# Kernel optimization log

Hardware: AMD Instinct MI355X
Metric: run time of the kernel (lower is better)

## Reference

```python
import jax, jax.numpy as jnp
import numpy as np

N_NODES = 100000


def sage_conv(x, src, dst, W_l, b_l, W_r):
    # PyG SAGEConv (aggr='mean'): out = lin_l(mean_j x_j) + lin_r(x_i)
    msg = x[src]  # [E, d] gather of source-node features
    agg = jax.ops.segment_sum(msg, dst, num_segments=N_NODES)  # [N, d]
    deg = jax.ops.segment_sum(jnp.ones((src.shape[0],), x.dtype), dst,
                              num_segments=N_NODES)
    mean = agg / jnp.clip(deg, 1.0, None)[:, None]
    return mean @ W_l.T + b_l + x @ W_r.T


def setup_inputs() -> dict:
    key = jax.random.key(0)
    ks = jax.random.split(key, 12)
    d_in, d_h, d_out, n_edges = 64, 64, 2, 1200000
    s = 1.0 / np.sqrt(d_h)
    inp = {
        "x": jax.random.normal(ks[0], (N_NODES, d_in), dtype=jnp.float32),
        "edge_index": jax.random.randint(ks[1], (2, n_edges), 0, N_NODES,
                                         dtype=jnp.int64),
        "W_l1": jax.random.uniform(ks[2], (d_h, d_in), jnp.float32, -s, s),
        "b_l1": jax.random.uniform(ks[3], (d_h,), jnp.float32, -s, s),
        "W_r1": jax.random.uniform(ks[4], (d_h, d_in), jnp.float32, -s, s),
        "W_l2": jax.random.uniform(ks[5], (d_h, d_h), jnp.float32, -s, s),
        "b_l2": jax.random.uniform(ks[6], (d_h,), jnp.float32, -s, s),
        "W_r2": jax.random.uniform(ks[7], (d_h, d_h), jnp.float32, -s, s),
        "W_c": jax.random.uniform(ks[8], (d_out, d_h), jnp.float32, -s, s),
        "b_c": jax.random.uniform(ks[9], (d_out,), jnp.float32, -s, s),
    }
    return inp


def reference(x, edge_index, W_l1, b_l1, W_r1, W_l2, b_l2, W_r2, W_c, b_c):
    src, dst = edge_index[0], edge_index[1]
    # layer 1 + relu (dropout is identity in eval mode)
    h = jax.nn.relu(sage_conv(x, src, dst, W_l1, b_l1, W_r1))
    # layer 2 (no relu per forward())
    h = sage_conv(h, src, dst, W_l2, b_l2, W_r2)
    # classifier
    return h @ W_c.T + b_c
```

## Files before the change

### kernel.cpp

```cpp
#include <hip/hip_runtime.h>

#define N_NODES 100000
#define D 64
#define NTILES 3125
#define NBUCK 391
#define NBLK_A 256
#define GCNT_N (NBUCK * NBLK_A)
#define NCHUNK ((GCNT_N + 255) / 256)
#define NTILE_T (N_NODES / 32)
#define TROW 72
#define TBLK 512

typedef __attribute__((ext_vector_type(8))) short short8;
typedef __attribute__((ext_vector_type(16))) float f32x16;
union Pack8 { uint4 u; short8 s; };

__device__ __forceinline__ unsigned f2bf(float f) {
  unsigned u = __float_as_uint(f);
  return (u + 0x7fffu + ((u >> 16) & 1u)) >> 16;
}
#define BF_LO(u) __uint_as_float(((unsigned)(u)) << 16)
#define BF_HI(u) __uint_as_float(((unsigned)(u)) & 0xffff0000u)


__global__ __launch_bounds__(256) void passA_count(const int* __restrict__ dst,
                                                   int* __restrict__ gcnt,
                                                   int nE, int ec) {
  __shared__ int cnt[NBUCK];
  int t = threadIdx.x, blk = blockIdx.x;
  for (int i = t; i < NBUCK; i += 256) cnt[i] = 0;
  __syncthreads();
  int e0 = blk * ec, e1 = min(e0 + ec, nE);
  for (int e = e0 + t; e < e1; e += 256) atomicAdd(&cnt[dst[e] >> 8], 1);
  __syncthreads();
  for (int b = t; b < NBUCK; b += 256) gcnt[b * NBLK_A + blk] = cnt[b];
}

__global__ void gscan_p1(const int* __restrict__ g, int* __restrict__ csum) {
  int t = threadIdx.x, b = blockIdx.x;
  int i = b * 256 + t;
  int v = (i < GCNT_N) ? g[i] : 0;
  for (int off = 32; off; off >>= 1) v += __shfl_down(v, off);
  __shared__ int ws4[4];
  if ((t & 63) == 0) ws4[t >> 6] = v;
  __syncthreads();
  if (t == 0) csum[b] = ws4[0] + ws4[1] + ws4[2] + ws4[3];
}

__global__ void gscan_p2(int* __restrict__ csum, int nB) {
  __shared__ int s[1024];
  int t = threadIdx.x;
  int orig = (t < nB) ? csum[t] : 0;
  s[t] = orig;
  __syncthreads();
  for (int off = 1; off < 1024; off <<= 1) {
    int v = (t >= off) ? s[t - off] : 0;
    __syncthreads();
    s[t] += v;
    __syncthreads();
  }
  if (t < nB) csum[t] = s[t] - orig;
}

__global__ void gscan_p3(int* __restrict__ g, const int* __restrict__ csum) {
  __shared__ int s[256];
  int t = threadIdx.x, b = blockIdx.x;
  int i = b * 256 + t;
  int d = (i < GCNT_N) ? g[i] : 0;
  s[t] = d;
  __syncthreads();
  for (int off = 1; off < 256; off <<= 1) {
    int v = (t >= off) ? s[t - off] : 0;
    __syncthreads();
    s[t] += v;
    __syncthreads();
  }
  if (i < GCNT_N) g[i] = s[t] - d + csum[b];
}

__global__ __launch_bounds__(256) void passC_prep(
    const int* __restrict__ src, const int* __restrict__ dst,
    const int* __restrict__ S, uint2* __restrict__ pairs, int nE, int ec,
    const float* __restrict__ Wc, const float* __restrict__ Wl2,
    const float* __restrict__ Wr2, const float* __restrict__ bl2,
    const float* __restrict__ bc, const float* __restrict__ Wl1,
    const float* __restrict__ Wr1, float* __restrict__ A2,
    float* __restrict__ B2, float* __restrict__ bfv,
    unsigned short* __restrict__ wcat) {
  __shared__ int cur[NBUCK];
  int t = threadIdx.x, blk = blockIdx.x;
  if (blk < NBLK_A) {
    for (int b = t; b < NBUCK; b += 256) cur[b] = S[b * NBLK_A + blk];
    __syncthreads();
    int e0 = blk * ec, e1 = min(e0 + ec, nE);
    for (int e = e0 + t; e < e1; e += 256) {
      int d = dst[e];
      int p = atomicAdd(&cur[d >> 8], 1);
      pairs[p] = make_uint2((unsigned)d, (unsigned)src[e]);
    }
  } else {
    for (int i = t; i < 8192; i += 256)
      wcat[i] = (unsigned short)f2bf((i < 4096) ? Wl1[i] : Wr1[i - 4096]);
    if (t < 128) {
      int c = t >> 6, k = t & 63;
      float sa = 0.f, sb = 0.f;
      for (int j = 0; j < 64; ++j) {
        float w = Wc[c * 64 + j];
        sa = fmaf(w, Wl2[j * 64 + k], sa);
        sb = fmaf(w, Wr2[j * 64 + k], sb);
      }
      A2[c * 64 + k] = sa;
      B2[c * 64 + k] = sb;
    }
    if (t < 2) {
      float s = bc[t];
      for (int j = 0; j < 64; ++j) s = fmaf(Wc[t * 64 + j], bl2[j], s);
      bfv[t] = s;
    }
  }
}

__global__ __launch_bounds__(256) void passD_transform(
    const uint2* __restrict__ pairs, const int* __restrict__ S,
    int* __restrict__ rowstart, int* __restrict__ degI,
    uint2* __restrict__ srt, int nE,
    const float* __restrict__ x, const unsigned short* __restrict__ wcat,
    const float* __restrict__ bl, unsigned short* __restrict__ t1,
    unsigned short* __restrict__ r1b) {
  __shared__ int lh[256];
  __shared__ int sc[256];
  __shared__ int cur[256];
  int t = threadIdx.x;
  if (blockIdx.x < NBUCK) {
    int b = blockIdx.x;
    int base = S[b * NBLK_A];
    int end = (b == NBUCK - 1) ? nE : S[(b + 1) * NBLK_A];
    lh[t] = 0;
    __syncthreads();
    for (int p = base + t; p < end; p += 256) atomicAdd(&lh[pairs[p].x & 255], 1);
    __syncthreads();
    int d = lh[t];
    sc[t] = d;
    __syncthreads();
    for (int off = 1; off < 256; off <<= 1) {
      int v = (t >= off) ? sc[t - off] : 0;
      __syncthreads();
      sc[t] += v;
      __syncthreads();
    }
    int ex = sc[t] - d;
    int node = b * 256 + t;
    if (node < N_NODES) {
      rowstart[node] = base + ex;
      degI[node] = d;
    }
    cur[t] = base + ex;
    __syncthreads();
    for (int p = base + t; p < end; p += 256) {
      uint2 e = pairs[p];
      int slot = atomicAdd(&cur[e.x & 255], 1);
      srt[slot] = e;
    }
  } else {
    int lane = t & 63;
    int l31 = lane & 31, hi = lane >> 5;

    short8 af[4][4];
#pragma unroll
    for (int jt = 0; jt < 4; ++jt)
#pragma unroll
      for (int kk = 0; kk < 4; ++kk)
        af[jt][kk] =
            *(const short8*)(wcat + (jt * 32 + l31) * 64 + kk * 16 + 8 * hi);

    const f32x16 Z = {0.f, 0.f, 0.f, 0.f, 0.f, 0.f, 0.f, 0.f,
                      0.f, 0.f, 0.f, 0.f, 0.f, 0.f, 0.f, 0.f};
    const float4* x4 = (const float4*)x;

    int gw = ((blockIdx.x - NBUCK) * 256 + t) >> 6;
    int nW = (TBLK * 256) >> 6;

    for (int tile = gw; tile < NTILE_T; tile += nW) {
      int node = tile * 32 + l31;
      f32x16 acc[4] = {Z, Z, Z, Z};
#pragma unroll
      for (int kk = 0; kk < 4; ++kk) {
        float4 fa = x4[(size_t)node * 16 + kk * 4 + 2 * hi];
        float4 fb = x4[(size_t)node * 16 + kk * 4 + 2 * hi + 1];
        Pack8 pk;
        pk.u.x = f2bf(fa.x) | (f2bf(fa.y) << 16);
        pk.u.y = f2bf(fa.z) | (f2bf(fa.w) << 16);
        pk.u.z = f2bf(fb.x) | (f2bf(fb.y) << 16);
        pk.u.w = f2bf(fb.z) | (f2bf(fb.w) << 16);
        acc[0] = __builtin_amdgcn_mfma_f32_32x32x16_bf16(af[0][kk], pk.s, acc[0], 0, 0, 0);
        acc[1] = __builtin_amdgcn_mfma_f32_32x32x16_bf16(af[1][kk], pk.s, acc[1], 0, 0, 0);
        acc[2] = __builtin_amdgcn_mfma_f32_32x32x16_bf16(af[2][kk], pk.s, acc[2], 0, 0, 0);
        acc[3] = __builtin_amdgcn_mfma_f32_32x32x16_bf16(af[3][kk], pk.s, acc[3], 0, 0, 0);
      }
#pragma unroll
      for (int jt = 0; jt < 2; ++jt)
#pragma unroll
        for (int rg = 0; rg < 4; ++rg) {
          int j0 = jt * 32 + 8 * rg + 4 * hi;
          uint2 p;
          p.x = f2bf(acc[jt][4 * rg + 0]) | (f2bf(acc[jt][4 * rg + 1]) << 16);
          p.y = f2bf(acc[jt][4 * rg + 2]) | (f2bf(acc[jt][4 * rg + 3]) << 16);
          *(uint2*)(t1 + (size_t)node * 64 + j0) = p;
        }
#pragma unroll
      for (int jt = 2; jt < 4; ++jt)
#pragma unroll
        for (int rg = 0; rg < 4; ++rg) {
          int j0 = (jt - 2) * 32 + 8 * rg + 4 * hi;
          float4 bv = ((const float4*)bl)[j0 >> 2];
          uint2 p;
          p.x = f2bf(acc[jt][4 * rg + 0] + bv.x) |
                (f2bf(acc[jt][4 * rg + 1] + bv.y) << 16);
          p.y = f2bf(acc[jt][4 * rg + 2] + bv.z) |
                (f2bf(acc[jt][4 * rg + 3] + bv.w) << 16);
          *(uint2*)(r1b + (size_t)node * 64 + j0) = p;
        }
    }
  }
}

__global__ __launch_bounds__(256) void tile_g1(
    const uint2* __restrict__ srt, const int* __restrict__ rowstart,
    const unsigned short* __restrict__ t1,
    const unsigned short* __restrict__ r1b, const float* __restrict__ A2,
    const float* __restrict__ B2, float2* __restrict__ g2,
    float2* __restrict__ s2, int nE) {
  __shared__ float pAB[4][64];
  __shared__ unsigned short stg[4][2][16 * TROW];
  __shared__ int ideg[4][64];
  int t = threadIdx.x, lane = t & 63, w = t >> 6;
  pAB[t >> 6][t & 63] = (t < 128) ? A2[t] : B2[t - 128];
  __syncthreads();

  int tile = blockIdx.x;
  int base = rowstart[tile * 32];
  int end = (tile == NTILES - 1) ? nE : rowstart[(tile + 1) * 32];
  int l31 = lane & 31, hi = lane >> 5;
  int o = lane >> 3, j8 = lane & 7;
  unsigned short* stA = &stg[w][0][0];
  unsigned short* stB = &stg[w][1][0];

  int ngAll = (end > base) ? ((end - base + 15) >> 4) : 0;
  int gper = (ngAll + 3) >> 2;
  int wbase = base + min(w * gper, ngAll) * 16;
  int wend = min(base + min((w + 1) * gper, ngAll) * 16, end);

  const f32x16 Z = {0.f, 0.f, 0.f, 0.f, 0.f, 0.f, 0.f, 0.f,
                    0.f, 0.f, 0.f, 0.f, 0.f, 0.f, 0.f, 0.f};
  f32x16 acc0 = Z, acc1 = Z;
  int degc = 0;
  int ng = (wend > wbase) ? ((wend - wbase + 15) >> 4) : 0;

  uint2 prA = make_uint2(0u, 0u), prB = make_uint2(0u, 0u);
  int cntA = 0, cntB = 0;
  uint4 vA0 = make_uint4(0, 0, 0, 0), vA1 = vA0, vB0 = vA0, vB1 = vA0;
  if (ng > 0) {
    prA = srt[min(wbase + (lane & 15), nE - 1)];
    cntA = min(wend - wbase, 16);
    int s0 = __shfl((int)prA.y, o), s1 = __shfl((int)prA.y, 8 + o);
    vA0 = *(const uint4*)(t1 + (size_t)((o < cntA) ? s0 : 0) * 64 + j8 * 8);
    vA1 = *(const uint4*)(t1 + (size_t)((8 + o < cntA) ? s1 : 0) * 64 + j8 * 8);
  }
  if (ng > 1) {
    int nb = wbase + 16;
    prB = srt[min(nb + (lane & 15), nE - 1)];
    cntB = min(wend - nb, 16);
    int s0 = __shfl((int)prB.y, o), s1 = __shfl((int)prB.y, 8 + o);
    vB0 = *(const uint4*)(t1 + (size_t)((o < cntB) ? s0 : 0) * 64 + j8 * 8);
    vB1 = *(const uint4*)(t1 + (size_t)((8 + o < cntB) ? s1 : 0) * 64 + j8 * 8);
  }

  for (int gg = 0; gg < ng; gg += 2) {
    bool hasB = (gg + 1 < ng);
    *(uint4*)(stA + o * TROW + j8 * 8) = vA0;
    *(uint4*)(stA + (8 + o) * TROW + j8 * 8) = vA1;
    if (hasB) {
      *(uint4*)(stB + o * TROW + j8 * 8) = vB0;
      *(uint4*)(stB + (8 + o) * TROW + j8 * 8) = vB1;
    }
    unsigned amA[8], amB[8];
#pragma unroll
    for (int m = 0; m < 8; ++m) {
      int e = 8 * hi + m;
      int dv = __shfl((int)prA.x, e);
      bool ok = (e < cntA) && ((dv & 31) == l31);
      amA[m] = ok ? 0x3F80u : 0u;
      degc += (amA[m] >> 7) & 1;
    }
    if (hasB) {
#pragma unroll
      for (int m = 0; m < 8; ++m) {
        int e = 8 * hi + m;
        int dv = __shfl((int)prB.x, e);
        bool ok = (e < cntB) && ((dv & 31) == l31);
        amB[m] = ok ? 0x3F80u : 0u;
        degc += (amB[m] >> 7) & 1;
      }
    }
    if (gg + 2 < ng) {
      int nb = wbase + (gg + 2) * 16;
      prA = srt[min(nb + (lane & 15), nE - 1)];
      cntA = min(wend - nb, 16);
      int s0 = __shfl((int)prA.y, o), s1 = __shfl((int)prA.y, 8 + o);
      vA0 = *(const uint4*)(t1 + (size_t)((o < cntA) ? s0 : 0) * 64 + j8 * 8);
      vA1 = *(const uint4*)(t1 + (size_t)((8 + o < cntA) ? s1 : 0) * 64 + j8 * 8);
    }
    if (gg + 3 < ng) {
      int nb = wbase + (gg + 3) * 16;
      prB = srt[min(nb + (lane & 15), nE - 1)];
      cntB = min(wend - nb, 16);
      int s0 = __shfl((int)prB.y, o), s1 = __shfl((int)prB.y, 8 + o);
      vB0 = *(const uint4*)(t1 + (size_t)((o < cntB) ? s0 : 0) * 64 + j8 * 8);
      vB1 = *(const uint4*)(t1 + (size_t)((8 + o < cntB) ? s1 : 0) * 64 + j8 * 8);
    }
    {
      Pack8 I;
      I.u.x = amA[0] | (amA[1] << 16);
      I.u.y = amA[2] | (amA[3] << 16);
      I.u.z = amA[4] | (amA[5] << 16);
      I.u.w = amA[6] | (amA[7] << 16);
      unsigned short b0[8], b1[8];
#pragma unroll
      for (int m = 0; m < 8; ++m) {
        b0[m] = stA[(8 * hi + m) * TROW + l31];
        b1[m] = stA[(8 * hi + m) * TROW + 32 + l31];
      }
      Pack8 F0, F1;
      F0.u.x = b0[0] | ((unsigned)b0[1] << 16);
      F0.u.y = b0[2] | ((unsigned)b0[3] << 16);
      F0.u.z = b0[4] | ((unsigned)b0[5] << 16);
      F0.u.w = b0[6] | ((unsigned)b0[7] << 16);
      F1.u.x = b1[0] | ((unsigned)b1[1] << 16);
      F1.u.y = b1[2] | ((unsigned)b1[3] << 16);
      F1.u.z = b1[4] | ((unsigned)b1[5] << 16);
      F1.u.w = b1[6] | ((unsigned)b1[7] << 16);
      acc0 = __builtin_amdgcn_mfma_f32_32x32x16_bf16(F0.s, I.s, acc0, 0, 0, 0);
      acc1 = __builtin_amdgcn_mfma_f32_32x32x16_bf16(F1.s, I.s, acc1, 0, 0, 0);
    }
    if (hasB) {
      Pack8 I;
      I.u.x = amB[0] | (amB[1] << 16);
      I.u.y = amB[2] | (amB[3] << 16);
      I.u.z = amB[4] | (amB[5] << 16);
      I.u.w = amB[6] | (amB[7] << 16);
      unsigned short b0[8], b1[8];
#pragma unroll
      for (int m = 0; m < 8; ++m) {
        b0[m] = stB[(8 * hi + m) * TROW + l31];
        b1[m] = stB[(8 * hi + m) * TROW + 32 + l31];
      }
      Pack8 F0, F1;
      F0.u.x = b0[0] | ((unsigned)b0[1] << 16);
      F0.u.y = b0[2] | ((unsigned)b0[3] << 16);
      F0.u.z = b0[4] | ((unsigned)b0[5] << 16);
      F0.u.w = b0[6] | ((unsigned)b0[7] << 16);
      F1.u.x = b1[0] | ((unsigned)b1[1] << 16);
      F1.u.y = b1[2] | ((unsigned)b1[3] << 16);
      F1.u.z = b1[4] | ((unsigned)b1[5] << 16);
      F1.u.w = b1[6] | ((unsigned)b1[7] << 16);
      acc0 = __builtin_amdgcn_mfma_f32_32x32x16_bf16(F0.s, I.s, acc0, 0, 0, 0);
      acc1 = __builtin_amdgcn_mfma_f32_32x32x16_bf16(F1.s, I.s, acc1, 0, 0, 0);
    }
  }

  ideg[w][lane] = degc;
  __syncthreads();
  float* red = (float*)&stg[0][0][0];
  for (int r = 1; r < 4; ++r) {
    if (w == r) {
#pragma unroll
      for (int i = 0; i < 16; ++i) {
        red[i * 64 + lane] = acc0[i];
        red[(16 + i) * 64 + lane] = acc1[i];
      }
    }
    __syncthreads();
    if (w == 0) {
#pragma unroll
      for (int i = 0; i < 16; ++i) {
        acc0[i] += red[i * 64 + lane];
        acc1[i] += red[(16 + i) * 64 + lane];
      }
    }
    __syncthreads();
  }

  if (w == 0) {
    int dtot = ideg[0][lane] + ideg[1][lane] + ideg[2][lane] + ideg[3][lane];
    float degf = (float)(dtot + __shfl_xor(dtot, 32));
    float inv = 1.f / fmaxf(degf, 1.f);
    int node = tile * 32 + l31;
    float d0 = 0.f, d1 = 0.f, d2 = 0.f, d3 = 0.f;
#pragma unroll
    for (int fb = 0; fb < 2; ++fb) {
#pragma unroll
      for (int q4 = 0; q4 < 4; ++q4) {
        int f0 = fb * 32 + q4 * 8 + 4 * hi;
        uint2 rv = *(const uint2*)(r1b + (size_t)node * 64 + f0);
        float bias[4] = {BF_LO(rv.x), BF_HI(rv.x), BF_LO(rv.y), BF_HI(rv.y)};
#pragma unroll
        for (int j = 0; j < 4; ++j) {
          float a = fb ? acc1[q4 * 4 + j] : acc0[q4 * 4 + j];
          float hv = fmaxf(fmaf(a, inv, bias[j]), 0.f);
          int f = f0 + j;
          d0 = fmaf(hv, pAB[0][f], d0);
          d1 = fmaf(hv, pAB[1][f], d1);
          d2 = fmaf(hv, pAB[2][f], d2);
          d3 = fmaf(hv, pAB[3][f], d3);
        }
      }
    }
    d0 += __shfl_xor(d0, 32);
    d1 += __shfl_xor(d1, 32);
    d2 += __shfl_xor(d2, 32);
    d3 += __shfl_xor(d3, 32);
    if (hi == 0) {
      g2[node] = make_float2(d0, d1);
      s2[node] = make_float2(d2, d3);
    }
  }
}

__global__ __launch_bounds__(256) void gather2_kernel(
    const int* __restrict__ rowstart, const int* __restrict__ degI,
    const uint2* __restrict__ srt, const float2* __restrict__ g2,
    const float2* __restrict__ s2, const float* __restrict__ bfv,
    float* __restrict__ out, int nE) {
  int tid = threadIdx.x, lane = tid & 63;
  int q = lane >> 4, l16 = lane & 15;
  float bf0 = bfv[0], bf1 = bfv[1];
  int gq = ((blockIdx.x * 256 + tid) >> 6) * 4 + q;
  int strideN = ((gridDim.x * 256) >> 6) * 4;
  for (int n = gq; n < N_NODES; n += strideN) {
    int rs = rowstart[n], dg = degI[n];
    float s0 = 0.f, s1 = 0.f;
    for (int base = 0; base < dg; base += 16) {
      int e = base + l16;
      int a = (int)srt[min(rs + ((e < dg) ? e : 0), nE - 1)].y;
      float2 v = g2[a];
      float m = (e < dg) ? 1.f : 0.f;
      s0 = fmaf(v.x, m, s0);
      s1 = fmaf(v.y, m, s1);
    }
    s0 += __shfl_xor(s0, 1); s0 += __shfl_xor(s0, 2);
    s0 += __shfl_xor(s0, 4); s0 += __shfl_xor(s0, 8);
    s1 += __shfl_xor(s1, 1); s1 += __shfl_xor(s1, 2);
    s1 += __shfl_xor(s1, 4); s1 += __shfl_xor(s1, 8);
    if (l16 == 0) {
      float inv = 1.f / (float)max(dg, 1);
      float2 sv = s2[n];
      out[(size_t)n * 2 + 0] = fmaf(s0, inv, sv.x) + bf0;
      out[(size_t)n * 2 + 1] = fmaf(s1, inv, sv.y) + bf1;
    }
  }
}

extern "C" void kernel_launch(void* const* d_in, const int* in_sizes, int n_in,
                              void* d_out, int out_size, void* d_ws,
                              size_t ws_size, hipStream_t stream) {
  const float* x   = (const float*)d_in[0];
  const int*   ei  = (const int*)d_in[1];
  const float* Wl1 = (const float*)d_in[2];
  const float* bl1 = (const float*)d_in[3];
  const float* Wr1 = (const float*)d_in[4];
  const float* Wl2 = (const float*)d_in[5];
  const float* bl2 = (const float*)d_in[6];
  const float* Wr2 = (const float*)d_in[7];
  const float* Wc  = (const float*)d_in[8];
  const float* bc  = (const float*)d_in[9];
  float* out = (float*)d_out;

  int nE = in_sizes[1] / 2;
  const int* src = ei;
  const int* dst = ei + nE;

  uint2* pairs = (uint2*)d_ws;
  uint2* srt = pairs + nE;
  unsigned short* t1 = (unsigned short*)(srt + nE);
  unsigned short* r1b = t1 + (size_t)N_NODES * D;
  float2* g2 = (float2*)(r1b + (size_t)N_NODES * D);
  float2* s2 = g2 + N_NODES;
  float* A2 = (float*)(s2 + N_NODES);
  float* B2 = A2 + 128;
  float* bfv = B2 + 128;
  unsigned short* wcat = (unsigned short*)(bfv + 4);
  int* degI = (int*)(wcat + 8192);
  int* rowstart = degI + N_NODES;
  int* gcnt = rowstart + N_NODES;
  int* csum = gcnt + GCNT_N;

  int ec = (nE + NBLK_A - 1) / NBLK_A;

  passA_count<<<NBLK_A, 256, 0, stream>>>(dst, gcnt, nE, ec);
  gscan_p1<<<NCHUNK, 256, 0, stream>>>(gcnt, csum);
  gscan_p2<<<1, 1024, 0, stream>>>(csum, NCHUNK);
  gscan_p3<<<NCHUNK, 256, 0, stream>>>(gcnt, csum);
  passC_prep<<<NBLK_A + 1, 256, 0, stream>>>(src, dst, gcnt, pairs, nE, ec,
                                             Wc, Wl2, Wr2, bl2, bc, Wl1, Wr1,
                                             A2, B2, bfv, wcat);
  passD_transform<<<NBUCK + TBLK, 256, 0, stream>>>(pairs, gcnt, rowstart,
                                                    degI, srt, nE, x, wcat,
                                                    bl1, t1, r1b);
  tile_g1<<<NTILES, 256, 0, stream>>>(srt, rowstart, t1, r1b, A2, B2, g2, s2,
                                      nE);
  gather2_kernel<<<512, 256, 0, stream>>>(rowstart, degI, srt, g2, s2, bfv,
                                          out, nE);
}
```

Measured before the change: 131.1 us.

## Pack edge pairs into 32-bit words and replace per-node CSR with 32-node tile bins

Edges are packed as one 32-bit word (low-8 destination bits in the top byte, source index in the low 24 bits), halving the traffic of the pairs and sorted-edge buffers. The second-level sort in passD now only bins edges into eight 32-node tiles instead of a full 256-way per-node counting sort, dropping the per-node rowstart/degree arrays. The final layer-2 gather becomes a per-bucket kernel that accumulates with shared-memory float atomics over the unsorted bucket pairs. This cuts memory traffic and scan work, at the cost of more LDS atomic contention and summation order that is no longer deterministic.

```diff
diff --git a/kernel.cpp b/kernel.cpp
--- a/kernel.cpp
+++ b/kernel.cpp
@@ -23,6 +23,7 @@
 #define BF_HI(u) __uint_as_float(((unsigned)(u)) & 0xffff0000u)
 
 
+
 __global__ __launch_bounds__(256) void passA_count(const int* __restrict__ dst,
                                                    int* __restrict__ gcnt,
                                                    int nE, int ec) {
@@ -80,7 +81,7 @@
 
 __global__ __launch_bounds__(256) void passC_prep(
     const int* __restrict__ src, const int* __restrict__ dst,
-    const int* __restrict__ S, uint2* __restrict__ pairs, int nE, int ec,
+    const int* __restrict__ S, unsigned* __restrict__ pairs4, int nE, int ec,
     const float* __restrict__ Wc, const float* __restrict__ Wl2,
     const float* __restrict__ Wr2, const float* __restrict__ bl2,
     const float* __restrict__ bc, const float* __restrict__ Wl1,
@@ -96,7 +97,7 @@
     for (int e = e0 + t; e < e1; e += 256) {
       int d = dst[e];
       int p = atomicAdd(&cur[d >> 8], 1);
-      pairs[p] = make_uint2((unsigned)d, (unsigned)src[e]);
+      pairs4[p] = ((unsigned)(d & 255) << 24) | (unsigned)src[e];
     }
   } else {
     for (int i = t; i < 8192; i += 256)
@@ -121,45 +122,45 @@
 }
 
 __global__ __launch_bounds__(256) void passD_transform(
-    const uint2* __restrict__ pairs, const int* __restrict__ S,
-    int* __restrict__ rowstart, int* __restrict__ degI,
-    uint2* __restrict__ srt, int nE,
+    const unsigned* __restrict__ pairs4, const int* __restrict__ S,
+    int* __restrict__ tstart, unsigned* __restrict__ srt4, int nE,
     const float* __restrict__ x, const unsigned short* __restrict__ wcat,
     const float* __restrict__ bl, unsigned short* __restrict__ t1,
     unsigned short* __restrict__ r1b) {
-  __shared__ int lh[256];
-  __shared__ int sc[256];
-  __shared__ int cur[256];
+  __shared__ int h8[8 * 16];
+  __shared__ int ex8[9];
+  __shared__ int cur8[8];
   int t = threadIdx.x;
   if (blockIdx.x < NBUCK) {
     int b = blockIdx.x;
     int base = S[b * NBLK_A];
     int end = (b == NBUCK - 1) ? nE : S[(b + 1) * NBLK_A];
-    lh[t] = 0;
-    __syncthreads();
-    for (int p = base + t; p < end; p += 256) atomicAdd(&lh[pairs[p].x & 255], 1);
-    __syncthreads();
-    int d = lh[t];
-    sc[t] = d;
-    __syncthreads();
-    for (int off = 1; off < 256; off <<= 1) {
-      int v = (t >= off) ? sc[t - off] : 0;
-      __syncthreads();
-      sc[t] += v;
-      __syncthreads();
-    }
-    int ex = sc[t] - d;
-    int node = b * 256 + t;
-    if (node < N_NODES) {
-      rowstart[node] = base + ex;
-      degI[node] = d;
-    }
-    cur[t] = base + ex;
+    if (t < 128) h8[t] = 0;
+    __syncthreads();
+    for (int p = base + t; p < end; p += 256)
+      atomicAdd(&h8[((pairs4[p] >> 29) & 7) * 16 + (t & 15)], 1);
+    __syncthreads();
+    if (t == 0) {
+      int run = base;
+      for (int bin = 0; bin < 8; ++bin) {
+        ex8[bin] = run;
+        int s = 0;
+        for (int i = 0; i < 16; ++i) s += h8[bin * 16 + i];
+        run += s;
+      }
+      ex8[8] = run;
+    }
+    __syncthreads();
+    if (t < 8) {
+      cur8[t] = ex8[t];
+      tstart[b * 8 + t] = ex8[t];
+    }
+    if (b == NBUCK - 1 && t == 0) tstart[NBUCK * 8] = nE;
     __syncthreads();
     for (int p = base + t; p < end; p += 256) {
-      uint2 e = pairs[p];
-      int slot = atomicAdd(&cur[e.x & 255], 1);
-      srt[slot] = e;
+      unsigned pk = pairs4[p];
+      int slot = atomicAdd(&cur8[(pk >> 29) & 7], 1);
+      srt4[slot] = pk;
     }
   } else {
     int lane = t & 63;
@@ -225,7 +226,7 @@
 }
 
 __global__ __launch_bounds__(256) void tile_g1(
-    const uint2* __restrict__ srt, const int* __restrict__ rowstart,
+    const unsigned* __restrict__ srt4, const int* __restrict__ tstart,
     const unsigned short* __restrict__ t1,
     const unsigned short* __restrict__ r1b, const float* __restrict__ A2,
     const float* __restrict__ B2, float2* __restrict__ g2,
@@ -238,8 +239,8 @@
   __syncthreads();
 
   int tile = blockIdx.x;
-  int base = rowstart[tile * 32];
-  int end = (tile == NTILES - 1) ? nE : rowstart[(tile + 1) * 32];
+  int base = tstart[tile];
+  int end = tstart[tile + 1];
   int l31 = lane & 31, hi = lane >> 5;
   int o = lane >> 3, j8 = lane & 7;
   unsigned short* stA = &stg[w][0][0];
@@ -256,21 +257,23 @@
   int degc = 0;
   int ng = (wend > wbase) ? ((wend - wbase + 15) >> 4) : 0;
 
-  uint2 prA = make_uint2(0u, 0u), prB = make_uint2(0u, 0u);
+  unsigned pkA = 0u, pkB = 0u;
   int cntA = 0, cntB = 0;
   uint4 vA0 = make_uint4(0, 0, 0, 0), vA1 = vA0, vB0 = vA0, vB1 = vA0;
   if (ng > 0) {
-    prA = srt[min(wbase + (lane & 15), nE - 1)];
+    pkA = srt4[min(wbase + (lane & 15), nE - 1)];
     cntA = min(wend - wbase, 16);
-    int s0 = __shfl((int)prA.y, o), s1 = __shfl((int)prA.y, 8 + o);
+    int s0 = __shfl((int)pkA, o) & 0xFFFFFF;
+    int s1 = __shfl((int)pkA, 8 + o) & 0xFFFFFF;
     vA0 = *(const uint4*)(t1 + (size_t)((o < cntA) ? s0 : 0) * 64 + j8 * 8);
     vA1 = *(const uint4*)(t1 + (size_t)((8 + o < cntA) ? s1 : 0) * 64 + j8 * 8);
   }
   if (ng > 1) {
     int nb = wbase + 16;
-    prB = srt[min(nb + (lane & 15), nE - 1)];
+    pkB = srt4[min(nb + (lane & 15), nE - 1)];
     cntB = min(wend - nb, 16);
-    int s0 = __shfl((int)prB.y, o), s1 = __shfl((int)prB.y, 8 + o);
+    int s0 = __shfl((int)pkB, o) & 0xFFFFFF;
+    int s1 = __shfl((int)pkB, 8 + o) & 0xFFFFFF;
     vB0 = *(const uint4*)(t1 + (size_t)((o < cntB) ? s0 : 0) * 64 + j8 * 8);
     vB1 = *(const uint4*)(t1 + (size_t)((8 + o < cntB) ? s1 : 0) * 64 + j8 * 8);
   }
@@ -287,8 +290,8 @@
 #pragma unroll
     for (int m = 0; m < 8; ++m) {
       int e = 8 * hi + m;
-      int dv = __shfl((int)prA.x, e);
-      bool ok = (e < cntA) && ((dv & 31) == l31);
+      int pv = __shfl((int)pkA, e);
+      bool ok = (e < cntA) && (((pv >> 24) & 31) == l31);
       amA[m] = ok ? 0x3F80u : 0u;
       degc += (amA[m] >> 7) & 1;
     }
@@ -296,25 +299,27 @@
 #pragma unroll
       for (int m = 0; m < 8; ++m) {
         int e = 8 * hi + m;
-        int dv = __shfl((int)prB.x, e);
-        bool ok = (e < cntB) && ((dv & 31) == l31);
+        int pv = __shfl((int)pkB, e);
+        bool ok = (e < cntB) && (((pv >> 24) & 31) == l31);
         amB[m] = ok ? 0x3F80u : 0u;
         degc += (amB[m] >> 7) & 1;
       }
     }
     if (gg + 2 < ng) {
       int nb = wbase + (gg + 2) * 16;
-      prA = srt[min(nb + (lane & 15), nE - 1)];
+      pkA = srt4[min(nb + (lane & 15), nE - 1)];
       cntA = min(wend - nb, 16);
-      int s0 = __shfl((int)prA.y, o), s1 = __shfl((int)prA.y, 8 + o);
+      int s0 = __shfl((int)pkA, o) & 0xFFFFFF;
+      int s1 = __shfl((int)pkA, 8 + o) & 0xFFFFFF;
       vA0 = *(const uint4*)(t1 + (size_t)((o < cntA) ? s0 : 0) * 64 + j8 * 8);
       vA1 = *(const uint4*)(t1 + (size_t)((8 + o < cntA) ? s1 : 0) * 64 + j8 * 8);
     }
     if (gg + 3 < ng) {
       int nb = wbase + (gg + 3) * 16;
-      prB = srt[min(nb + (lane & 15), nE - 1)];
+      pkB = srt4[min(nb + (lane & 15), nE - 1)];
       cntB = min(wend - nb, 16);
-      int s0 = __shfl((int)prB.y, o), s1 = __shfl((int)prB.y, 8 + o);
+      int s0 = __shfl((int)pkB, o) & 0xFFFFFF;
+      int s1 = __shfl((int)pkB, 8 + o) & 0xFFFFFF;
       vB0 = *(const uint4*)(t1 + (size_t)((o < cntB) ? s0 : 0) * 64 + j8 * 8);
       vB1 = *(const uint4*)(t1 + (size_t)((8 + o < cntB) ? s1 : 0) * 64 + j8 * 8);
     }
@@ -426,37 +431,34 @@
   }
 }
 
-__global__ __launch_bounds__(256) void gather2_kernel(
-    const int* __restrict__ rowstart, const int* __restrict__ degI,
-    const uint2* __restrict__ srt, const float2* __restrict__ g2,
-    const float2* __restrict__ s2, const float* __restrict__ bfv,
-    float* __restrict__ out, int nE) {
-  int tid = threadIdx.x, lane = tid & 63;
-  int q = lane >> 4, l16 = lane & 15;
-  float bf0 = bfv[0], bf1 = bfv[1];
-  int gq = ((blockIdx.x * 256 + tid) >> 6) * 4 + q;
-  int strideN = ((gridDim.x * 256) >> 6) * 4;
-  for (int n = gq; n < N_NODES; n += strideN) {
-    int rs = rowstart[n], dg = degI[n];
-    float s0 = 0.f, s1 = 0.f;
-    for (int base = 0; base < dg; base += 16) {
-      int e = base + l16;
-      int a = (int)srt[min(rs + ((e < dg) ? e : 0), nE - 1)].y;
-      float2 v = g2[a];
-      float m = (e < dg) ? 1.f : 0.f;
-      s0 = fmaf(v.x, m, s0);
-      s1 = fmaf(v.y, m, s1);
-    }
-    s0 += __shfl_xor(s0, 1); s0 += __shfl_xor(s0, 2);
-    s0 += __shfl_xor(s0, 4); s0 += __shfl_xor(s0, 8);
-    s1 += __shfl_xor(s1, 1); s1 += __shfl_xor(s1, 2);
-    s1 += __shfl_xor(s1, 4); s1 += __shfl_xor(s1, 8);
-    if (l16 == 0) {
-      float inv = 1.f / (float)max(dg, 1);
-      float2 sv = s2[n];
-      out[(size_t)n * 2 + 0] = fmaf(s0, inv, sv.x) + bf0;
-      out[(size_t)n * 2 + 1] = fmaf(s1, inv, sv.y) + bf1;
-    }
+__global__ __launch_bounds__(256) void bucket_g2(
+    const unsigned* __restrict__ pairs4, const int* __restrict__ S,
+    const float2* __restrict__ g2, const float2* __restrict__ s2,
+    const float* __restrict__ bfv, float* __restrict__ out, int nE) {
+  __shared__ float o0[256], o1[256];
+  __shared__ int cnt[256];
+  int t = threadIdx.x, b = blockIdx.x;
+  o0[t] = 0.f;
+  o1[t] = 0.f;
+  cnt[t] = 0;
+  __syncthreads();
+  int base = S[b * NBLK_A];
+  int end = (b == NBUCK - 1) ? nE : S[(b + 1) * NBLK_A];
+  for (int p = base + t; p < end; p += 256) {
+    unsigned pk = pairs4[p];
+    float2 v = g2[pk & 0xFFFFFFu];
+    int dl = pk >> 24;
+    atomicAdd(&o0[dl], v.x);
+    atomicAdd(&o1[dl], v.y);
+    atomicAdd(&cnt[dl], 1);
+  }
+  __syncthreads();
+  int node = b * 256 + t;
+  if (node < N_NODES) {
+    float inv = 1.f / (float)max(cnt[t], 1);
+    float2 sv = s2[node];
+    out[(size_t)node * 2 + 0] = fmaf(o0[t], inv, sv.x) + bfv[0];
+    out[(size_t)node * 2 + 1] = fmaf(o1[t], inv, sv.y) + bfv[1];
   }
 }
 
@@ -479,9 +481,9 @@
   const int* src = ei;
   const int* dst = ei + nE;
 
-  uint2* pairs = (uint2*)d_ws;
-  uint2* srt = pairs + nE;
-  unsigned short* t1 = (unsigned short*)(srt + nE);
+  unsigned* pairs4 = (unsigned*)d_ws;
+  unsigned* srt4 = pairs4 + nE;
+  unsigned short* t1 = (unsigned short*)(srt4 + nE);
   unsigned short* r1b = t1 + (size_t)N_NODES * D;
   float2* g2 = (float2*)(r1b + (size_t)N_NODES * D);
   float2* s2 = g2 + N_NODES;
@@ -489,9 +491,8 @@
   float* B2 = A2 + 128;
   float* bfv = B2 + 128;
   unsigned short* wcat = (unsigned short*)(bfv + 4);
-  int* degI = (int*)(wcat + 8192);
-  int* rowstart = degI + N_NODES;
-  int* gcnt = rowstart + N_NODES;
+  int* tstart = (int*)(wcat + 8192);
+  int* gcnt = tstart + (NBUCK * 8 + 2);
   int* csum = gcnt + GCNT_N;
 
   int ec = (nE + NBLK_A - 1) / NBLK_A;
@@ -500,14 +501,13 @@
   gscan_p1<<<NCHUNK, 256, 0, stream>>>(gcnt, csum);
   gscan_p2<<<1, 1024, 0, stream>>>(csum, NCHUNK);
   gscan_p3<<<NCHUNK, 256, 0, stream>>>(gcnt, csum);
-  passC_prep<<<NBLK_A + 1, 256, 0, stream>>>(src, dst, gcnt, pairs, nE, ec,
+  passC_prep<<<NBLK_A + 1, 256, 0, stream>>>(src, dst, gcnt, pairs4, nE, ec,
                                              Wc, Wl2, Wr2, bl2, bc, Wl1, Wr1,
                                              A2, B2, bfv, wcat);
-  passD_transform<<<NBUCK + TBLK, 256, 0, stream>>>(pairs, gcnt, rowstart,
-                                                    degI, srt, nE, x, wcat,
-                                                    bl1, t1, r1b);
-  tile_g1<<<NTILES, 256, 0, stream>>>(srt, rowstart, t1, r1b, A2, B2, g2, s2,
+  passD_transform<<<NBUCK + TBLK, 256, 0, stream>>>(pairs4, gcnt, tstart,
+                                                    srt4, nE, x, wcat, bl1,
+                                                    t1, r1b);
+  tile_g1<<<NTILES, 256, 0, stream>>>(srt4, tstart, t1, r1b, A2, B2, g2, s2,
                                       nE);
-  gather2_kernel<<<512, 256, 0, stream>>>(rowstart, degI, srt, g2, s2, bfv,
-                                          out, nE);
-}
+  bucket_g2<<<NBUCK, 256, 0, stream>>>(pairs4, gcnt, g2, s2, bfv, out, nE);
+}
```

Result: faster. 124.5 us (median of 2 runs) (-5.0%).
